# Performance work log

Measured on AMD Instinct MI355X. Metric: run time of the kernel, lower is better.

Reference implementation:

```python
import jax, jax.numpy as jnp
import numpy as np

N, H, E, T, ED, AB = 50000, 64, 800000, 800000, 64, 16


def setup_inputs() -> dict:
    key = jax.random.key(0)
    ks = jax.random.split(key, 26)

    def nrm(k, shape, scale=1.0):
        return jax.random.normal(k, shape, dtype=jnp.float32) * scale

    d = {}
    d["s"] = nrm(ks[0], (N, H))
    d["v"] = nrm(ks[1], (N, H, 3))
    d["edge_index"] = jax.random.randint(ks[2], (2, E), 0, N, dtype=jnp.int32)
    d["edge_rbf"] = jax.random.uniform(ks[3], (E, ED), dtype=jnp.float32)
    raw_dir = jax.random.normal(ks[4], (E, 3), dtype=jnp.float32)
    d["edge_dir"] = raw_dir / jnp.linalg.norm(raw_dir, axis=-1, keepdims=True)
    d["triplet_kj"] = jax.random.randint(ks[5], (T,), 0, E, dtype=jnp.int32)
    d["triplet_ji"] = jax.random.randint(ks[6], (T,), 0, E, dtype=jnp.int32)
    d["angle_feat"] = jax.random.uniform(ks[7], (T, AB), dtype=jnp.float32)

    def lin(kw, kb, fan_in, fan_out):
        sc = 1.0 / np.sqrt(fan_in)
        return nrm(kw, (fan_in, fan_out), sc), nrm(kb, (fan_out,), sc)

    d["W_t1"], d["b_t1"] = lin(ks[8], ks[9], 2 * ED + AB, H)
    d["W_t2"], d["b_t2"] = lin(ks[10], ks[11], H, H)
    d["W_m1"], d["b_m1"] = lin(ks[12], ks[13], 2 * H + ED + H, H)
    d["W_m2"], d["b_m2"] = lin(ks[14], ks[15], H, 2 * H)
    d["W_u1"], d["b_u1"] = lin(ks[16], ks[17], 3 * H, H)
    d["W_u2"], d["b_u2"] = lin(ks[18], ks[19], H, H)
    d["W_g1"], d["b_g1"] = lin(ks[20], ks[21], 3 * H, H)
    d["W_g2"], d["b_g2"] = lin(ks[22], ks[23], H, H)
    d["ln_g"] = jnp.ones((H,), jnp.float32)
    d["ln_b"] = jnp.zeros((H,), jnp.float32)
    return d


def _mlp(x, W1, b1, W2, b2):
    return jax.nn.silu(x @ W1 + b1) @ W2 + b2


def reference(s, v, edge_index, edge_rbf, edge_dir, triplet_kj, triplet_ji,
              angle_feat, W_t1, b_t1, W_t2, b_t2, W_m1, b_m1, W_m2, b_m2,
              W_u1, b_u1, W_u2, b_u2, W_g1, b_g1, W_g2, b_g2, ln_g, ln_b):
    n_nodes, hid = s.shape
    n_edges = edge_rbf.shape[0]

    # 3-body triplet messages: gather two edge rbf rows + angle feature
    t_in = jnp.concatenate([edge_rbf[triplet_kj], edge_rbf[triplet_ji], angle_feat], axis=-1)
    t_msg = _mlp(t_in, W_t1, b_t1, W_t2, b_t2)                 # [T, H]
    angle_agg = jax.ops.segment_sum(t_msg, triplet_ji, num_segments=n_edges)  # [E, H]

    src, dst = edge_index[0], edge_index[1]
    msg_in = jnp.concatenate([s[src], s[dst], edge_rbf, angle_agg], axis=-1)  # [E, 4H]
    msg = _mlp(msg_in, W_m1, b_m1, W_m2, b_m2)                 # [E, 2H]
    m_s, m_v_coeff = jnp.split(msg, 2, axis=-1)

    agg_s = jax.ops.segment_sum(m_s, dst, num_segments=n_nodes)  # [N, H]
    m_v = m_v_coeff[:, :, None] * edge_dir[:, None, :]          # [E, H, 3]
    agg_v = jax.ops.segment_sum(m_v.reshape(n_edges, hid * 3), dst,
                                num_segments=n_nodes).reshape(n_nodes, hid, 3)

    v_norm = jnp.linalg.norm(v, axis=-1)                        # [N, H]
    ctx = jnp.concatenate([s, agg_s, v_norm], axis=-1)          # [N, 3H]
    s_new = s + _mlp(ctx, W_u1, b_u1, W_u2, b_u2)
    gate = jax.nn.sigmoid(_mlp(ctx, W_g1, b_g1, W_g2, b_g2))
    v_new = v + gate[..., None] * agg_v

    mu = s_new.mean(axis=-1, keepdims=True)
    var = s_new.var(axis=-1, keepdims=True)
    s_ln = (s_new - mu) / jnp.sqrt(var + 1e-5) * ln_g + ln_b
    s_out = jax.nn.silu(s_ln)
    return (s_out, v_new)
```

## Files before the change

### kernel.cpp

```cpp
#include <hip/hip_runtime.h>
#include <cstdint>
#include <cstddef>

#define NN 50000
#define NE 800000
#define NT 800000

typedef unsigned short u16;
typedef unsigned int u32;
typedef __attribute__((ext_vector_type(8))) short short8;
typedef __attribute__((ext_vector_type(4))) float f32x4;

__device__ __forceinline__ float silu_f(float x) { return x / (1.f + __expf(-x)); }
__device__ __forceinline__ float sigm_f(float x) { return 1.f / (1.f + __expf(-x)); }
__device__ __forceinline__ u16 f2b(float x) {
  u32 u = __float_as_uint(x);
  u32 r = u + 0x7fffu + ((u >> 16) & 1u);
  return (u16)(r >> 16);
}
__device__ __forceinline__ float b2f(u16 h) { return __uint_as_float(((u32)h) << 16); }

template <int RW>
__device__ __forceinline__ int lx(int r, int c) {
  return r * RW + ((((c >> 3) ^ (r & 7)) << 3) | (c & 7));
}

__global__ __launch_bounds__(256) void kcvt2(const float* __restrict__ erbf,
                                             u16* __restrict__ erbf_bf,
                                             const float* __restrict__ s,
                                             u16* __restrict__ s_bf) {
  int i = blockIdx.x * 256 + threadIdx.x;
  const float* in;
  u16* out;
  int j;
  if (i < NE * 16) { in = erbf; out = erbf_bf; j = i; }
  else { j = i - NE * 16; if (j >= NN * 16) return; in = s; out = s_bf; }
  float4 v = ((const float4*)in)[j];
  uint2 p;
  p.x = (u32)f2b(v.x) | ((u32)f2b(v.y) << 16);
  p.y = (u32)f2b(v.z) | ((u32)f2b(v.w) << 16);
  ((uint2*)out)[j] = p;
}

__global__ __launch_bounds__(256) void khist2(const int* __restrict__ tji,
                                              const int* __restrict__ edst,
                                              int* __restrict__ tcnt,
                                              int* __restrict__ ncnt) {
  int i = blockIdx.x * 256 + threadIdx.x;
  if (i < NT) atomicAdd(&tcnt[tji[i]], 1);
  else {
    int j = i - NT;
    if (j < NE) atomicAdd(&ncnt[edst[j]], 1);
  }
}

__global__ __launch_bounds__(256) void kscan1b(
    const int* __restrict__ inA, int nA, int* __restrict__ outA, int* __restrict__ bsA, int BA,
    const int* __restrict__ inB, int nB, int* __restrict__ outB, int* __restrict__ bsB) {
  __shared__ int sh[256];
  const int* in; int n; int* out; int* bs; int blk;
  if ((int)blockIdx.x < BA) { in = inA; n = nA; out = outA; bs = bsA; blk = blockIdx.x; }
  else { in = inB; n = nB; out = outB; bs = bsB; blk = blockIdx.x - BA; }
  int tid = threadIdx.x;
  size_t base = (size_t)blk * 1024;
  int v[4];
  int acc = 0;
#pragma unroll
  for (int q = 0; q < 4; ++q) {
    size_t i = base + (size_t)tid * 4 + q;
    int x = (i < (size_t)n) ? in[i] : 0;
    v[q] = acc;
    acc += x;
  }
  sh[tid] = acc;
  __syncthreads();
  for (int off = 1; off < 256; off <<= 1) {
    int y = (tid >= off) ? sh[tid - off] : 0;
    __syncthreads();
    sh[tid] += y;
    __syncthreads();
  }
  int excl = (tid == 0) ? 0 : sh[tid - 1];
  if (tid == 255) bs[blk] = sh[255];
#pragma unroll
  for (int q = 0; q < 4; ++q) {
    size_t i = base + (size_t)tid * 4 + q;
    if (i < (size_t)n) out[i] = excl + v[q];
  }
}

__global__ __launch_bounds__(1024) void kscan2b(int* __restrict__ bsA, int nbA,
                                                int* __restrict__ bsB, int nbB) {
  __shared__ int sh[1024];
  int* bs = (blockIdx.x == 0) ? bsA : bsB;
  int nb = (blockIdx.x == 0) ? nbA : nbB;
  int tid = threadIdx.x;
  sh[tid] = (tid < nb) ? bs[tid] : 0;
  __syncthreads();
  for (int off = 1; off < 1024; off <<= 1) {
    int y = (tid >= off) ? sh[tid - off] : 0;
    __syncthreads();
    sh[tid] += y;
    __syncthreads();
  }
  if (tid < nb) bs[tid] = (tid == 0) ? 0 : sh[tid - 1];
}

__global__ __launch_bounds__(256) void kscan3b(
    int* __restrict__ outA, const int* __restrict__ bsA, int nA, int totalA,
    int* __restrict__ outB, const int* __restrict__ bsB, int nB, int totalB) {
  int i = blockIdx.x * 256 + threadIdx.x;
  if (i <= nA) {
    if (i < nA) outA[i] += bsA[i >> 10];
    else outA[nA] = totalA;
  } else {
    int j = i - (nA + 1);
    if (j < nB) outB[j] += bsB[j >> 10];
    else if (j == nB) outB[nB] = totalB;
  }
}

__global__ __launch_bounds__(256) void kscatter_inv_afeat(
    const int* __restrict__ keys, const int* __restrict__ off, int n,
    int* __restrict__ cnt, int* __restrict__ tids,
    const float* __restrict__ afeat, u16* __restrict__ afeat_s) {
  int i = blockIdx.x * 256 + threadIdx.x;
  if (i < n) {
    int k = keys[i];
    int slot = off[k] + (atomicSub(&cnt[k], 1) - 1);
    tids[slot] = i;
    const float4* src = (const float4*)(afeat + (size_t)i * 16);
    uint2* dst = (uint2*)(afeat_s + (size_t)slot * 16);
#pragma unroll
    for (int q = 0; q < 4; ++q) {
      float4 v = src[q];
      uint2 p;
      p.x = (u32)f2b(v.x) | ((u32)f2b(v.y) << 16);
      p.y = (u32)f2b(v.z) | ((u32)f2b(v.w) << 16);
      dst[q] = p;
    }
  }
}

__global__ __launch_bounds__(256) void kscatter_fwd_dir(const int* __restrict__ keys,
                                                        const int* __restrict__ off, int n,
                                                        int* __restrict__ cnt,
                                                        int* __restrict__ eids,
                                                        const float* __restrict__ dir,
                                                        float* __restrict__ dir_s) {
  int i = blockIdx.x * 256 + threadIdx.x;
  if (i < n) {
    int k = keys[i];
    int slot = off[k] + (atomicSub(&cnt[k], 1) - 1);
    eids[slot] = i;
    dir_s[(size_t)slot * 3 + 0] = dir[(size_t)i * 3 + 0];
    dir_s[(size_t)slot * 3 + 1] = dir[(size_t)i * 3 + 1];
    dir_s[(size_t)slot * 3 + 2] = dir[(size_t)i * 3 + 2];
  }
}

__global__ __launch_bounds__(256) void kprepw_all(
    const float* __restrict__ Wt1, const float* __restrict__ Wt2,
    const float* __restrict__ Wm1, const float* __restrict__ Wm2,
    const float* __restrict__ Wu1, const float* __restrict__ Wu2,
    const float* __restrict__ Wg1, const float* __restrict__ Wg2,
    u16* __restrict__ Pt1, u16* __restrict__ Pt2,
    u16* __restrict__ Pm1, u16* __restrict__ Pm2,
    u16* __restrict__ Pu1, u16* __restrict__ Pu2,
    u16* __restrict__ Pg1, u16* __restrict__ Pg2) {
  int gid = blockIdx.x * 256 + threadIdx.x;
  int f = gid >> 6, l = gid & 63;
  const float* W; u16* out; int K, N, fl;
  if (f < 20)       { W = Wt1; out = Pt1; K = 144; N = 64;  fl = f; }
  else if (f < 28)  { W = Wt2; out = Pt2; K = 64;  N = 64;  fl = f - 20; }
  else if (f < 60)  { W = Wm1; out = Pm1; K = 256; N = 64;  fl = f - 28; }
  else if (f < 76)  { W = Wm2; out = Pm2; K = 64;  N = 128; fl = f - 60; }
  else if (f < 100) { W = Wu1; out = Pu1; K = 192; N = 64;  fl = f - 76; }
  else if (f < 108) { W = Wu2; out = Pu2; K = 64;  N = 64;  fl = f - 100; }
  else if (f < 132) { W = Wg1; out = Pg1; K = 192; N = 64;  fl = f - 108; }
  else if (f < 140) { W = Wg2; out = Pg2; K = 64;  N = 64;  fl = f - 132; }
  else return;
  int nt = fl % (N / 16);
  int kt = fl / (N / 16);
  int k0 = kt * 32 + (l >> 4) * 8;
  int n = nt * 16 + (l & 15);
  u16 vals[8];
#pragma unroll
  for (int j = 0; j < 8; ++j) {
    int kk = k0 + j;
    vals[j] = (kk < K) ? f2b(W[(size_t)kk * N + n]) : (u16)0;
  }
  uint4* dst = (uint4*)(out + (size_t)fl * 512 + l * 8);
  uint4 p;
  p.x = (u32)vals[0] | ((u32)vals[1] << 16);
  p.y = (u32)vals[2] | ((u32)vals[3] << 16);
  p.z = (u32)vals[4] | ((u32)vals[5] << 16);
  p.w = (u32)vals[6] | ((u32)vals[7] << 16);
  *dst = p;
}

__global__ __launch_bounds__(256) void ktrip_mfma(
    const int* __restrict__ tkj, const int* __restrict__ tji,
    const u16* __restrict__ erbf_bf, const u16* __restrict__ afeat_s,
    const int* __restrict__ tids,
    const u16* __restrict__ Wp1, const float* __restrict__ b1,
    const u16* __restrict__ Wp2, const float* __restrict__ b2,
    u16* __restrict__ tmsg_s) {
  __shared__ u16 Xs[64 * 192];
  __shared__ u16 Hs[64 * 64];
  const int tid = threadIdx.x;
  const int l = tid & 63;
  const int w = tid >> 6;
  const int st0 = blockIdx.x * 64;

#pragma unroll
  for (int it = 0; it < 4; ++it) {
    int idx = it * 256 + tid;
    int sel = idx >> 9, r = (idx >> 3) & 63, ch = idx & 7;
    int t = tids[st0 + r];
    int node = sel ? tji[t] : tkj[t];
    uint4 vv = *(const uint4*)&erbf_bf[(size_t)node * 64 + ch * 8];
    *(uint4*)&Xs[lx<192>(r, sel * 64 + ch * 8)] = vv;
  }
  {
    int r = tid >> 2, c = (tid & 3) * 4;
    uint2 p2 = *(const uint2*)&afeat_s[(size_t)(st0 + r) * 16 + c];
    *(uint2*)&Xs[lx<192>(r, 128 + c)] = p2;
  }
#pragma unroll
  for (int i = 0; i < 2; ++i) {
    int idx = i * 256 + tid;
    int r = idx >> 3, c = 144 + (idx & 7) * 2;
    *(u32*)&Xs[lx<192>(r, c)] = 0;
  }
  __syncthreads();

  f32x4 acc1[4];
  {
    float bias = b1[w * 16 + (l & 15)];
#pragma unroll
    for (int mt = 0; mt < 4; ++mt) acc1[mt] = (f32x4){bias, bias, bias, bias};
    for (int ks = 0; ks < 5; ++ks) {
      short8 bf = *(const short8*)(Wp1 + ((size_t)(ks * 4 + w) * 64 + l) * 8);
#pragma unroll
      for (int mt = 0; mt < 4; ++mt) {
        short8 af = *(const short8*)&Xs[lx<192>(mt * 16 + (l & 15), ks * 32 + ((l >> 4) << 3))];
        acc1[mt] = __builtin_amdgcn_mfma_f32_16x16x32_bf16(af, bf, acc1[mt], 0, 0, 0);
      }
    }
  }
#pragma unroll
  for (int mt = 0; mt < 4; ++mt)
#pragma unroll
    for (int q = 0; q < 4; ++q) {
      int r = mt * 16 + (l >> 4) * 4 + q;
      Hs[lx<64>(r, w * 16 + (l & 15))] = f2b(silu_f(acc1[mt][q]));
    }
  __syncthreads();

  f32x4 acc2[4];
  {
    float bias = b2[w * 16 + (l & 15)];
#pragma unroll
    for (int mt = 0; mt < 4; ++mt) acc2[mt] = (f32x4){bias, bias, bias, bias};
    for (int ks = 0; ks < 2; ++ks) {
      short8 bf = *(const short8*)(Wp2 + ((size_t)(ks * 4 + w) * 64 + l) * 8);
#pragma unroll
      for (int mt = 0; mt < 4; ++mt) {
        short8 af = *(const short8*)&Hs[lx<64>(mt * 16 + (l & 15), ks * 32 + ((l >> 4) << 3))];
        acc2[mt] = __builtin_amdgcn_mfma_f32_16x16x32_bf16(af, bf, acc2[mt], 0, 0, 0);
      }
    }
  }
  __syncthreads();
#pragma unroll
  for (int mt = 0; mt < 4; ++mt)
#pragma unroll
    for (int q = 0; q < 4; ++q) {
      int r = mt * 16 + (l >> 4) * 4 + q;
      Xs[lx<64>(r, w * 16 + (l & 15))] = f2b(acc2[mt][q]);
    }
  __syncthreads();
  for (int i = 0; i < 2; ++i) {
    int idx = i * 256 + tid;
    int r = idx >> 3, c0 = (idx & 7) << 3;
    uint4 val = *(const uint4*)&Xs[lx<64>(r, c0)];
    *(uint4*)(tmsg_s + (size_t)(st0 + r) * 64 + c0) = val;
  }
}

__global__ __launch_bounds__(256) void kmsg_mfma(
    const int* __restrict__ eidx, const u16* __restrict__ s_bf,
    const u16* __restrict__ erbf_bf,
    const int* __restrict__ toff, const u16* __restrict__ tmsg_s,
    const int* __restrict__ eids,
    const u16* __restrict__ Wp1, const float* __restrict__ b1,
    const u16* __restrict__ Wp2, const float* __restrict__ b2,
    u16* __restrict__ msg_s) {
  __shared__ u16 Xs[64 * 256];
  __shared__ u16 Hs[64 * 64];
  const int tid = threadIdx.x;
  const int l = tid & 63;
  const int w = tid >> 6;
  const int sl0 = blockIdx.x * 64;

#pragma unroll
  for (int i = 0; i < 2; ++i) {
    int idx = i * 256 + tid;
    int r = idx >> 3, c0 = (idx & 7) << 3;
    int e = eids[sl0 + r];
    uint4 vv = *(const uint4*)&erbf_bf[(size_t)e * 64 + c0];
    *(uint4*)&Xs[lx<256>(r, 128 + c0)] = vv;
  }
#pragma unroll
  for (int it = 0; it < 4; ++it) {
    int idx = it * 256 + tid;
    int sel = idx >> 9, r = (idx >> 3) & 63, ch = idx & 7;
    int e = eids[sl0 + r];
    int node = eidx[sel * NE + e];
    uint4 vv = *(const uint4*)&s_bf[(size_t)node * 64 + ch * 8];
    *(uint4*)&Xs[lx<256>(r, sel * 64 + ch * 8)] = vv;
  }
#pragma unroll
  for (int it = 0; it < 2; ++it) {
    int idx = it * 256 + tid;
    int r = idx >> 3, ch = idx & 7;
    int e = eids[sl0 + r];
    int r0 = toff[e], r1 = toff[e + 1];
    float a[8];
#pragma unroll
    for (int j = 0; j < 8; ++j) a[j] = 0.f;
    for (int ri = r0; ri < r1; ++ri) {
      uint4 pk = *(const uint4*)&tmsg_s[(size_t)ri * 64 + ch * 8];
      a[0] += b2f((u16)(pk.x & 0xffff)); a[1] += b2f((u16)(pk.x >> 16));
      a[2] += b2f((u16)(pk.y & 0xffff)); a[3] += b2f((u16)(pk.y >> 16));
      a[4] += b2f((u16)(pk.z & 0xffff)); a[5] += b2f((u16)(pk.z >> 16));
      a[6] += b2f((u16)(pk.w & 0xffff)); a[7] += b2f((u16)(pk.w >> 16));
    }
    uint4 p;
    p.x = (u32)f2b(a[0]) | ((u32)f2b(a[1]) << 16);
    p.y = (u32)f2b(a[2]) | ((u32)f2b(a[3]) << 16);
    p.z = (u32)f2b(a[4]) | ((u32)f2b(a[5]) << 16);
    p.w = (u32)f2b(a[6]) | ((u32)f2b(a[7]) << 16);
    *(uint4*)&Xs[lx<256>(r, 192 + ch * 8)] = p;
  }
  __syncthreads();

  f32x4 acc1[4];
  {
    float bias = b1[w * 16 + (l & 15)];
#pragma unroll
    for (int mt = 0; mt < 4; ++mt) acc1[mt] = (f32x4){bias, bias, bias, bias};
    for (int ks = 0; ks < 8; ++ks) {
      short8 bf = *(const short8*)(Wp1 + ((size_t)(ks * 4 + w) * 64 + l) * 8);
#pragma unroll
      for (int mt = 0; mt < 4; ++mt) {
        short8 af = *(const short8*)&Xs[lx<256>(mt * 16 + (l & 15), ks * 32 + ((l >> 4) << 3))];
        acc1[mt] = __builtin_amdgcn_mfma_f32_16x16x32_bf16(af, bf, acc1[mt], 0, 0, 0);
      }
    }
  }
#pragma unroll
  for (int mt = 0; mt < 4; ++mt)
#pragma unroll
    for (int q = 0; q < 4; ++q) {
      int r = mt * 16 + (l >> 4) * 4 + q;
      Hs[lx<64>(r, w * 16 + (l & 15))] = f2b(silu_f(acc1[mt][q]));
    }
  __syncthreads();

  f32x4 acc2[2][4];
#pragma unroll
  for (int pp = 0; pp < 2; ++pp) {
    int nt = w * 2 + pp;
    float bias = b2[nt * 16 + (l & 15)];
#pragma unroll
    for (int mt = 0; mt < 4; ++mt) acc2[pp][mt] = (f32x4){bias, bias, bias, bias};
    for (int ks = 0; ks < 2; ++ks) {
      short8 bf = *(const short8*)(Wp2 + ((size_t)(ks * 8 + nt) * 64 + l) * 8);
#pragma unroll
      for (int mt = 0; mt < 4; ++mt) {
        short8 af = *(const short8*)&Hs[lx<64>(mt * 16 + (l & 15), ks * 32 + ((l >> 4) << 3))];
        acc2[pp][mt] = __builtin_amdgcn_mfma_f32_16x16x32_bf16(af, bf, acc2[pp][mt], 0, 0, 0);
      }
    }
  }
  __syncthreads();
#pragma unroll
  for (int pp = 0; pp < 2; ++pp)
#pragma unroll
    for (int mt = 0; mt < 4; ++mt)
#pragma unroll
      for (int q = 0; q < 4; ++q) {
        int r = mt * 16 + (l >> 4) * 4 + q;
        Xs[lx<128>(r, (w * 2 + pp) * 16 + (l & 15))] = f2b(acc2[pp][mt][q]);
      }
  __syncthreads();
  for (int i = 0; i < 4; ++i) {
    int idx = i * 256 + tid;
    int r = idx >> 4, c0 = (idx & 15) << 3;
    uint4 val = *(const uint4*)&Xs[lx<128>(r, c0)];
    *(uint4*)(msg_s + (size_t)(sl0 + r) * 128 + c0) = val;
  }
}

__global__ __launch_bounds__(256) void kagg(
    const int* __restrict__ noff, const u16* __restrict__ msg_s,
    const float* __restrict__ dir_s,
    u16* __restrict__ aggs_bf, float* __restrict__ aggv) {
  const int lane = threadIdx.x & 63;
  const int wv = threadIdx.x >> 6;
  const int n = blockIdx.x * 4 + wv;
  if (n >= NN) return;
  const int r0 = noff[n], r1 = noff[n + 1];
  const int lrow = lane >> 4, lcol = lane & 15;
  const bool is_ms = (lcol < 8);

  float a[8];
  float v0[8], v1[8], v2[8];
#pragma unroll
  for (int j = 0; j < 8; ++j) { a[j] = 0.f; v0[j] = 0.f; v1[j] = 0.f; v2[j] = 0.f; }

  for (int r4 = r0; r4 < r1; r4 += 4) {
    int r = r4 + lrow;
    if (r < r1) {
      uint4 pk = *(const uint4*)&msg_s[(size_t)r * 128 + lcol * 8];
      float x[8];
      x[0] = b2f((u16)(pk.x & 0xffff)); x[1] = b2f((u16)(pk.x >> 16));
      x[2] = b2f((u16)(pk.y & 0xffff)); x[3] = b2f((u16)(pk.y >> 16));
      x[4] = b2f((u16)(pk.z & 0xffff)); x[5] = b2f((u16)(pk.z >> 16));
      x[6] = b2f((u16)(pk.w & 0xffff)); x[7] = b2f((u16)(pk.w >> 16));
      if (is_ms) {
#pragma unroll
        for (int j = 0; j < 8; ++j) a[j] += x[j];
      } else {
        float dx = dir_s[(size_t)r * 3 + 0];
        float dy = dir_s[(size_t)r * 3 + 1];
        float dz = dir_s[(size_t)r * 3 + 2];
#pragma unroll
        for (int j = 0; j < 8; ++j) {
          v0[j] += x[j] * dx; v1[j] += x[j] * dy; v2[j] += x[j] * dz;
        }
      }
    }
  }
#pragma unroll
  for (int j = 0; j < 8; ++j) {
    a[j] += __shfl_xor(a[j], 16);  a[j] += __shfl_xor(a[j], 32);
    v0[j] += __shfl_xor(v0[j], 16); v0[j] += __shfl_xor(v0[j], 32);
    v1[j] += __shfl_xor(v1[j], 16); v1[j] += __shfl_xor(v1[j], 32);
    v2[j] += __shfl_xor(v2[j], 16); v2[j] += __shfl_xor(v2[j], 32);
  }
  if (lrow == 0) {
    if (is_ms) {
      uint4 p;
      p.x = (u32)f2b(a[0]) | ((u32)f2b(a[1]) << 16);
      p.y = (u32)f2b(a[2]) | ((u32)f2b(a[3]) << 16);
      p.z = (u32)f2b(a[4]) | ((u32)f2b(a[5]) << 16);
      p.w = (u32)f2b(a[6]) | ((u32)f2b(a[7]) << 16);
      *(uint4*)&aggs_bf[(size_t)n * 64 + lcol * 8] = p;
    } else {
      int c0 = (lcol - 8) * 8;
      float* av = aggv + (size_t)n * 192 + (size_t)c0 * 3;
      float4 o0 = {v0[0], v1[0], v2[0], v0[1]};
      float4 o1 = {v1[1], v2[1], v0[2], v1[2]};
      float4 o2 = {v2[2], v0[3], v1[3], v2[3]};
      float4 o3 = {v0[4], v1[4], v2[4], v0[5]};
      float4 o4 = {v1[5], v2[5], v0[6], v1[6]};
      float4 o5 = {v2[6], v0[7], v1[7], v2[7]};
      float4* av4 = (float4*)av;
      av4[0] = o0; av4[1] = o1; av4[2] = o2; av4[3] = o3; av4[4] = o4; av4[5] = o5;
    }
  }
}

__global__ __launch_bounds__(256) void knode_mfma(
    const u16* __restrict__ s_bf, const float* __restrict__ v,
    const u16* __restrict__ aggs_bf, const float* __restrict__ aggv,
    const u16* __restrict__ WpU1, const float* __restrict__ bU1,
    const u16* __restrict__ WpU2, const float* __restrict__ bU2,
    const u16* __restrict__ WpG1, const float* __restrict__ bG1,
    const u16* __restrict__ WpG2, const float* __restrict__ bG2,
    const float* __restrict__ lng, const float* __restrict__ lnb,
    float* __restrict__ outs, float* __restrict__ outv) {
  __shared__ __align__(16) char smem[64 * 192 * 2 + 2 * 64 * 64 * 2];
  u16* Xs = (u16*)smem;
  u16* Hu = (u16*)(smem + 64 * 192 * 2);
  u16* Hg = Hu + 64 * 64;
  float* Fs = (float*)smem;

  const int tid = threadIdx.x;
  const int l = tid & 63;
  const int w = tid >> 6;
  const int n0 = blockIdx.x * 64;

  for (int i = 0; i < 2; ++i) {
    int idx = i * 256 + tid;
    int r = idx >> 3, c0 = (idx & 7) << 3;
    int nr = n0 + r; if (nr >= NN) nr = NN - 1;
    uint4 a = *(const uint4*)&s_bf[(size_t)nr * 64 + c0];
    *(uint4*)&Xs[lx<192>(r, c0)] = a;
    uint4 b = *(const uint4*)&aggs_bf[(size_t)nr * 64 + c0];
    *(uint4*)&Xs[lx<192>(r, 64 + c0)] = b;
  }
  for (int it = 0; it < 16; ++it) {
    int idx = it * 256 + tid;
    int r = idx >> 6, c = idx & 63;
    int nr = n0 + r; if (nr >= NN) nr = NN - 1;
    const float* vp = v + (size_t)nr * 192 + c * 3;
    float x = vp[0], y = vp[1], z = vp[2];
    Xs[lx<192>(r, 128 + c)] = f2b(sqrtf(x * x + y * y + z * z));
  }
  __syncthreads();

  f32x4 au[4], ag[4];
  {
    float biu = bU1[w * 16 + (l & 15)], big = bG1[w * 16 + (l & 15)];
#pragma unroll
    for (int mt = 0; mt < 4; ++mt) {
      au[mt] = (f32x4){biu, biu, biu, biu};
      ag[mt] = (f32x4){big, big, big, big};
    }
    for (int ks = 0; ks < 6; ++ks) {
      short8 bu = *(const short8*)(WpU1 + ((size_t)(ks * 4 + w) * 64 + l) * 8);
      short8 bg = *(const short8*)(WpG1 + ((size_t)(ks * 4 + w) * 64 + l) * 8);
#pragma unroll
      for (int mt = 0; mt < 4; ++mt) {
        short8 af = *(const short8*)&Xs[lx<192>(mt * 16 + (l & 15), ks * 32 + ((l >> 4) << 3))];
        au[mt] = __builtin_amdgcn_mfma_f32_16x16x32_bf16(af, bu, au[mt], 0, 0, 0);
        ag[mt] = __builtin_amdgcn_mfma_f32_16x16x32_bf16(af, bg, ag[mt], 0, 0, 0);
      }
    }
  }
#pragma unroll
  for (int mt = 0; mt < 4; ++mt)
#pragma unroll
    for (int q = 0; q < 4; ++q) {
      int r = mt * 16 + (l >> 4) * 4 + q;
      Hu[lx<64>(r, w * 16 + (l & 15))] = f2b(silu_f(au[mt][q]));
      Hg[lx<64>(r, w * 16 + (l & 15))] = f2b(silu_f(ag[mt][q]));
    }
  __syncthreads();

  f32x4 ou[4], og[4];
  {
    float biu = bU2[w * 16 + (l & 15)], big = bG2[w * 16 + (l & 15)];
#pragma unroll
    for (int mt = 0; mt < 4; ++mt) {
      ou[mt] = (f32x4){biu, biu, biu, biu};
      og[mt] = (f32x4){big, big, big, big};
    }
    for (int ks = 0; ks < 2; ++ks) {
      short8 bu = *(const short8*)(WpU2 + ((size_t)(ks * 4 + w) * 64 + l) * 8);
      short8 bg = *(const short8*)(WpG2 + ((size_t)(ks * 4 + w) * 64 + l) * 8);
#pragma unroll
      for (int mt = 0; mt < 4; ++mt) {
        short8 afu = *(const short8*)&Hu[lx<64>(mt * 16 + (l & 15), ks * 32 + ((l >> 4) << 3))];
        ou[mt] = __builtin_amdgcn_mfma_f32_16x16x32_bf16(afu, bu, ou[mt], 0, 0, 0);
        short8 afg = *(const short8*)&Hg[lx<64>(mt * 16 + (l & 15), ks * 32 + ((l >> 4) << 3))];
        og[mt] = __builtin_amdgcn_mfma_f32_16x16x32_bf16(afg, bg, og[mt], 0, 0, 0);
      }
    }
  }
#pragma unroll
  for (int mt = 0; mt < 4; ++mt)
#pragma unroll
    for (int q = 0; q < 4; ++q) {
      int r = mt * 16 + (l >> 4) * 4 + q;
      ou[mt][q] += b2f(Xs[lx<192>(r, w * 16 + (l & 15))]);
    }
  __syncthreads();

#pragma unroll
  for (int mt = 0; mt < 4; ++mt)
#pragma unroll
    for (int q = 0; q < 4; ++q) {
      int r = mt * 16 + (l >> 4) * 4 + q;
      Fs[r * 68 + w * 16 + (l & 15)] = ou[mt][q];
    }
  __syncthreads();
  {
    int r = tid >> 2, c0 = (tid & 3) * 16;
    float xv[16];
#pragma unroll
    for (int j4 = 0; j4 < 4; ++j4) {
      float4 t = *(const float4*)&Fs[r * 68 + c0 + j4 * 4];
      xv[j4 * 4 + 0] = t.x; xv[j4 * 4 + 1] = t.y;
      xv[j4 * 4 + 2] = t.z; xv[j4 * 4 + 3] = t.w;
    }
    float sm = 0.f, sq = 0.f;
#pragma unroll
    for (int j = 0; j < 16; ++j) { sm += xv[j]; sq += xv[j] * xv[j]; }
    sm += __shfl_xor(sm, 1); sq += __shfl_xor(sq, 1);
    sm += __shfl_xor(sm, 2); sq += __shfl_xor(sq, 2);
    float mu = sm * (1.f / 64.f);
    float var = sq * (1.f / 64.f) - mu * mu;
    float rstd = rsqrtf(var + 1e-5f);
    if (n0 + r < NN) {
      float* op = outs + (size_t)(n0 + r) * 64 + c0;
#pragma unroll
      for (int j4 = 0; j4 < 4; ++j4) {
        float4 o;
        float y0 = (xv[j4 * 4 + 0] - mu) * rstd * lng[c0 + j4 * 4 + 0] + lnb[c0 + j4 * 4 + 0];
        float y1 = (xv[j4 * 4 + 1] - mu) * rstd * lng[c0 + j4 * 4 + 1] + lnb[c0 + j4 * 4 + 1];
        float y2 = (xv[j4 * 4 + 2] - mu) * rstd * lng[c0 + j4 * 4 + 2] + lnb[c0 + j4 * 4 + 2];
        float y3 = (xv[j4 * 4 + 3] - mu) * rstd * lng[c0 + j4 * 4 + 3] + lnb[c0 + j4 * 4 + 3];
        o.x = silu_f(y0); o.y = silu_f(y1); o.z = silu_f(y2); o.w = silu_f(y3);
        *(float4*)(op + j4 * 4) = o;
      }
    }
  }
  __syncthreads();

#pragma unroll
  for (int mt = 0; mt < 4; ++mt)
#pragma unroll
    for (int q = 0; q < 4; ++q) {
      int r = mt * 16 + (l >> 4) * 4 + q;
      Fs[r * 68 + w * 16 + (l & 15)] = og[mt][q];
    }
  __syncthreads();
  {
    int r = tid >> 2, c0 = (tid & 3) * 16;
    int nr = n0 + r;
    if (nr < NN) {
      float gate[16];
#pragma unroll
      for (int j = 0; j < 16; ++j) gate[j] = sigm_f(Fs[r * 68 + c0 + j]);
      const float4* vp = (const float4*)(v + (size_t)nr * 192 + c0 * 3);
      const float4* ap = (const float4*)(aggv + (size_t)nr * 192 + c0 * 3);
      float4* op = (float4*)(outv + (size_t)nr * 192 + c0 * 3);
#pragma unroll
      for (int j4 = 0; j4 < 12; ++j4) {
        float4 vv = vp[j4], av = ap[j4], o;
        o.x = vv.x + gate[(j4 * 4 + 0) / 3] * av.x;
        o.y = vv.y + gate[(j4 * 4 + 1) / 3] * av.y;
        o.z = vv.z + gate[(j4 * 4 + 2) / 3] * av.z;
        o.w = vv.w + gate[(j4 * 4 + 3) / 3] * av.w;
        op[j4] = o;
      }
    }
  }
}

extern "C" void kernel_launch(void* const* d_in, const int* in_sizes, int n_in,
                              void* d_out, int out_size, void* d_ws, size_t ws_size,
                              hipStream_t stream) {
  const float* s     = (const float*)d_in[0];
  const float* v     = (const float*)d_in[1];
  const int*   eidx  = (const int*)d_in[2];
  const float* erbf  = (const float*)d_in[3];
  const float* edir  = (const float*)d_in[4];
  const int*   tkj   = (const int*)d_in[5];
  const int*   tji   = (const int*)d_in[6];
  const float* afeat = (const float*)d_in[7];
  const float* W_t1  = (const float*)d_in[8];
  const float* b_t1  = (const float*)d_in[9];
  const float* W_t2  = (const float*)d_in[10];
  const float* b_t2  = (const float*)d_in[11];
  const float* W_m1  = (const float*)d_in[12];
  const float* b_m1  = (const float*)d_in[13];
  const float* W_m2  = (const float*)d_in[14];
  const float* b_m2  = (const float*)d_in[15];
  const float* W_u1  = (const float*)d_in[16];
  const float* b_u1  = (const float*)d_in[17];
  const float* W_u2  = (const float*)d_in[18];
  const float* b_u2  = (const float*)d_in[19];
  const float* W_g1  = (const float*)d_in[20];
  const float* b_g1  = (const float*)d_in[21];
  const float* W_g2  = (const float*)d_in[22];
  const float* b_g2  = (const float*)d_in[23];
  const float* ln_g  = (const float*)d_in[24];
  const float* ln_b  = (const float*)d_in[25];

  char* w = (char*)d_ws;
  auto alloc = [&](size_t bytes) -> char* {
    char* p = w;
    w += (bytes + 255) & ~(size_t)255;
    return p;
  };
  int* toff  = (int*)alloc((size_t)(NE + 1) * 4);
  int* noff  = (int*)alloc((size_t)(NN + 1) * 4);
  int* tcnt  = (int*)alloc((size_t)NE * 4);
  int* ncnt  = (int*)alloc((size_t)NN * 4);
  int* tids  = (int*)alloc((size_t)NT * 4);
  int* eids  = (int*)alloc((size_t)NE * 4);
  int* bsum  = (int*)alloc(2048 * 4);
  float* dir_s = (float*)alloc((size_t)NE * 3 * 4);
  u16* msg_s  = (u16*)alloc((size_t)NE * 128 * 2);
  u16* tmsg_s = (u16*)alloc((size_t)NT * 64 * 2);
  u16* erbf_bf = (u16*)alloc((size_t)NE * 64 * 2);
  u16* s_bf    = (u16*)alloc((size_t)NN * 64 * 2);
  u16* Wp_t1 = (u16*)alloc((size_t)5 * 4 * 512 * 2);
  u16* Wp_t2 = (u16*)alloc((size_t)2 * 4 * 512 * 2);
  u16* Wp_m1 = (u16*)alloc((size_t)8 * 4 * 512 * 2);
  u16* Wp_m2 = (u16*)alloc((size_t)2 * 8 * 512 * 2);
  u16* Wp_u1 = (u16*)alloc((size_t)6 * 4 * 512 * 2);
  u16* Wp_u2 = (u16*)alloc((size_t)2 * 4 * 512 * 2);
  u16* Wp_g1 = (u16*)alloc((size_t)6 * 4 * 512 * 2);
  u16* Wp_g2 = (u16*)alloc((size_t)2 * 4 * 512 * 2);
  u16* afeat_s = msg_s;
  float* aggv = (float*)tmsg_s;
  u16* aggs_bf = tmsg_s + (size_t)NN * 384;

  hipMemsetAsync(tcnt, 0, (size_t)((char*)(ncnt + NN) - (char*)tcnt), stream);

  kcvt2<<<(NE * 16 + NN * 16 + 255) / 256, 256, 0, stream>>>(erbf, erbf_bf, s, s_bf);
  khist2<<<(NT + NE + 255) / 256, 256, 0, stream>>>(tji, eidx + NE, tcnt, ncnt);

  const int Bt = (NE + 1023) / 1024, Bn = (NN + 1023) / 1024;
  kscan1b<<<Bt + Bn, 256, 0, stream>>>(tcnt, NE, toff, bsum, Bt, ncnt, NN, noff, bsum + 1024);
  kscan2b<<<2, 1024, 0, stream>>>(bsum, Bt, bsum + 1024, Bn);
  kscan3b<<<(NE + 1 + NN + 1 + 255) / 256, 256, 0, stream>>>(toff, bsum, NE, NT,
                                                             noff, bsum + 1024, NN, NE);

  kscatter_inv_afeat<<<(NT + 255) / 256, 256, 0, stream>>>(tji, toff, NT, tcnt, tids,
                                                           afeat, afeat_s);
  kscatter_fwd_dir<<<(NE + 255) / 256, 256, 0, stream>>>(eidx + NE, noff, NE, ncnt, eids,
                                                         edir, dir_s);

  kprepw_all<<<35, 256, 0, stream>>>(W_t1, W_t2, W_m1, W_m2, W_u1, W_u2, W_g1, W_g2,
                                     Wp_t1, Wp_t2, Wp_m1, Wp_m2, Wp_u1, Wp_u2, Wp_g1, Wp_g2);

  ktrip_mfma<<<NT / 64, 256, 0, stream>>>(tkj, tji, erbf_bf, afeat_s, tids,
                                          Wp_t1, b_t1, Wp_t2, b_t2, tmsg_s);
  kmsg_mfma<<<NE / 64, 256, 0, stream>>>(eidx, s_bf, erbf_bf, toff, tmsg_s, eids,
                                         Wp_m1, b_m1, Wp_m2, b_m2, msg_s);
  kagg<<<(NN + 3) / 4, 256, 0, stream>>>(noff, msg_s, dir_s, aggs_bf, aggv);

  float* out_s = (float*)d_out;
  float* out_v = out_s + (size_t)NN * 64;
  knode_mfma<<<(NN + 63) / 64, 256, 0, stream>>>(s_bf, v, aggs_bf, aggv,
                                                 Wp_u1, b_u1, Wp_u2, b_u2,
                                                 Wp_g1, b_g1, Wp_g2, b_g2,
                                                 ln_g, ln_b, out_s, out_v);
}
```

Measured before the change: 643.5 us.

## Merge prep kernels and process edges in original order with scattered message writes

Fuses conversion with the histogram kernel, and merges the two scatter kernels with weight packing into one launch, cutting launch count. The message kernel now walks edges in their natural order, so its erbf/edge_index/toff reads are contiguous. It writes each output row to that edge's dst-sorted slot through a new eslot array, replacing the earlier gather through eids. This trades indirect reads for indirect 256-byte row writes.

New measurement: 618.1 us. 4.0% less time.

```diff
diff --git a/kernel.cpp b/kernel.cpp
--- a/kernel.cpp
+++ b/kernel.cpp
@@ -19,38 +19,38 @@
   return (u16)(r >> 16);
 }
 __device__ __forceinline__ float b2f(u16 h) { return __uint_as_float(((u32)h) << 16); }
+__device__ __forceinline__ u32 pk2(float a, float b) {
+  return (u32)f2b(a) | ((u32)f2b(b) << 16);
+}
 
 template <int RW>
 __device__ __forceinline__ int lx(int r, int c) {
   return r * RW + ((((c >> 3) ^ (r & 7)) << 3) | (c & 7));
 }
 
-__global__ __launch_bounds__(256) void kcvt2(const float* __restrict__ erbf,
-                                             u16* __restrict__ erbf_bf,
-                                             const float* __restrict__ s,
-                                             u16* __restrict__ s_bf) {
+__global__ __launch_bounds__(256) void kcvt_hist(
+    const float* __restrict__ erbf, u16* __restrict__ erbf_bf,
+    const float* __restrict__ s, u16* __restrict__ s_bf,
+    const int* __restrict__ tji, const int* __restrict__ edst,
+    int* __restrict__ tcnt, int* __restrict__ ncnt) {
   int i = blockIdx.x * 256 + threadIdx.x;
-  const float* in;
-  u16* out;
-  int j;
-  if (i < NE * 16) { in = erbf; out = erbf_bf; j = i; }
-  else { j = i - NE * 16; if (j >= NN * 16) return; in = s; out = s_bf; }
-  float4 v = ((const float4*)in)[j];
-  uint2 p;
-  p.x = (u32)f2b(v.x) | ((u32)f2b(v.y) << 16);
-  p.y = (u32)f2b(v.z) | ((u32)f2b(v.w) << 16);
-  ((uint2*)out)[j] = p;
-}
-
-__global__ __launch_bounds__(256) void khist2(const int* __restrict__ tji,
-                                              const int* __restrict__ edst,
-                                              int* __restrict__ tcnt,
-                                              int* __restrict__ ncnt) {
-  int i = blockIdx.x * 256 + threadIdx.x;
-  if (i < NT) atomicAdd(&tcnt[tji[i]], 1);
-  else {
-    int j = i - NT;
-    if (j < NE) atomicAdd(&ncnt[edst[j]], 1);
+  const int NCVT = (NE + NN) * 16;
+  if (i < NCVT) {
+    const float* in; u16* out; int j;
+    if (i < NE * 16) { in = erbf; out = erbf_bf; j = i; }
+    else { in = s; out = s_bf; j = i - NE * 16; }
+    float4 v = ((const float4*)in)[j];
+    uint2 p;
+    p.x = pk2(v.x, v.y);
+    p.y = pk2(v.z, v.w);
+    ((uint2*)out)[j] = p;
+  } else {
+    int j = i - NCVT;
+    if (j < NT) atomicAdd(&tcnt[tji[j]], 1);
+    else {
+      j -= NT;
+      if (j < NE) atomicAdd(&ncnt[edst[j]], 1);
+    }
   }
 }
 
@@ -120,46 +120,11 @@
   }
 }
 
-__global__ __launch_bounds__(256) void kscatter_inv_afeat(
-    const int* __restrict__ keys, const int* __restrict__ off, int n,
-    int* __restrict__ cnt, int* __restrict__ tids,
-    const float* __restrict__ afeat, u16* __restrict__ afeat_s) {
-  int i = blockIdx.x * 256 + threadIdx.x;
-  if (i < n) {
-    int k = keys[i];
-    int slot = off[k] + (atomicSub(&cnt[k], 1) - 1);
-    tids[slot] = i;
-    const float4* src = (const float4*)(afeat + (size_t)i * 16);
-    uint2* dst = (uint2*)(afeat_s + (size_t)slot * 16);
-#pragma unroll
-    for (int q = 0; q < 4; ++q) {
-      float4 v = src[q];
-      uint2 p;
-      p.x = (u32)f2b(v.x) | ((u32)f2b(v.y) << 16);
-      p.y = (u32)f2b(v.z) | ((u32)f2b(v.w) << 16);
-      dst[q] = p;
-    }
-  }
-}
-
-__global__ __launch_bounds__(256) void kscatter_fwd_dir(const int* __restrict__ keys,
-                                                        const int* __restrict__ off, int n,
-                                                        int* __restrict__ cnt,
-                                                        int* __restrict__ eids,
-                                                        const float* __restrict__ dir,
-                                                        float* __restrict__ dir_s) {
-  int i = blockIdx.x * 256 + threadIdx.x;
-  if (i < n) {
-    int k = keys[i];
-    int slot = off[k] + (atomicSub(&cnt[k], 1) - 1);
-    eids[slot] = i;
-    dir_s[(size_t)slot * 3 + 0] = dir[(size_t)i * 3 + 0];
-    dir_s[(size_t)slot * 3 + 1] = dir[(size_t)i * 3 + 1];
-    dir_s[(size_t)slot * 3 + 2] = dir[(size_t)i * 3 + 2];
-  }
-}
-
-__global__ __launch_bounds__(256) void kprepw_all(
+__global__ __launch_bounds__(256) void kprep_all(
+    const int* __restrict__ tji, const int* __restrict__ toff, int* __restrict__ tcnt,
+    int* __restrict__ tids, const float* __restrict__ afeat, u16* __restrict__ afeat_s,
+    const int* __restrict__ edst, const int* __restrict__ noff, int* __restrict__ ncnt,
+    int* __restrict__ eslot, const float* __restrict__ dir, float* __restrict__ dir_s,
     const float* __restrict__ Wt1, const float* __restrict__ Wt2,
     const float* __restrict__ Wm1, const float* __restrict__ Wm2,
     const float* __restrict__ Wu1, const float* __restrict__ Wu2,
@@ -168,35 +133,60 @@
     u16* __restrict__ Pm1, u16* __restrict__ Pm2,
     u16* __restrict__ Pu1, u16* __restrict__ Pu2,
     u16* __restrict__ Pg1, u16* __restrict__ Pg2) {
-  int gid = blockIdx.x * 256 + threadIdx.x;
-  int f = gid >> 6, l = gid & 63;
-  const float* W; u16* out; int K, N, fl;
-  if (f < 20)       { W = Wt1; out = Pt1; K = 144; N = 64;  fl = f; }
-  else if (f < 28)  { W = Wt2; out = Pt2; K = 64;  N = 64;  fl = f - 20; }
-  else if (f < 60)  { W = Wm1; out = Pm1; K = 256; N = 64;  fl = f - 28; }
-  else if (f < 76)  { W = Wm2; out = Pm2; K = 64;  N = 128; fl = f - 60; }
-  else if (f < 100) { W = Wu1; out = Pu1; K = 192; N = 64;  fl = f - 76; }
-  else if (f < 108) { W = Wu2; out = Pu2; K = 64;  N = 64;  fl = f - 100; }
-  else if (f < 132) { W = Wg1; out = Pg1; K = 192; N = 64;  fl = f - 108; }
-  else if (f < 140) { W = Wg2; out = Pg2; K = 64;  N = 64;  fl = f - 132; }
-  else return;
-  int nt = fl % (N / 16);
-  int kt = fl / (N / 16);
-  int k0 = kt * 32 + (l >> 4) * 8;
-  int n = nt * 16 + (l & 15);
-  u16 vals[8];
-#pragma unroll
-  for (int j = 0; j < 8; ++j) {
-    int kk = k0 + j;
-    vals[j] = (kk < K) ? f2b(W[(size_t)kk * N + n]) : (u16)0;
-  }
-  uint4* dst = (uint4*)(out + (size_t)fl * 512 + l * 8);
-  uint4 p;
-  p.x = (u32)vals[0] | ((u32)vals[1] << 16);
-  p.y = (u32)vals[2] | ((u32)vals[3] << 16);
-  p.z = (u32)vals[4] | ((u32)vals[5] << 16);
-  p.w = (u32)vals[6] | ((u32)vals[7] << 16);
-  *dst = p;
+  int i = blockIdx.x * 256 + threadIdx.x;
+  if (i < NT) {
+    int k = tji[i];
+    int slot = toff[k] + (atomicSub(&tcnt[k], 1) - 1);
+    tids[slot] = i;
+    const float4* src = (const float4*)(afeat + (size_t)i * 16);
+    uint2* dst = (uint2*)(afeat_s + (size_t)slot * 16);
+#pragma unroll
+    for (int q = 0; q < 4; ++q) {
+      float4 v = src[q];
+      uint2 p;
+      p.x = pk2(v.x, v.y);
+      p.y = pk2(v.z, v.w);
+      dst[q] = p;
+    }
+  } else if (i < NT + NE) {
+    int j = i - NT;
+    int k = edst[j];
+    int slot = noff[k] + (atomicSub(&ncnt[k], 1) - 1);
+    eslot[j] = slot;
+    dir_s[(size_t)slot * 3 + 0] = dir[(size_t)j * 3 + 0];
+    dir_s[(size_t)slot * 3 + 1] = dir[(size_t)j * 3 + 1];
+    dir_s[(size_t)slot * 3 + 2] = dir[(size_t)j * 3 + 2];
+  } else {
+    int g = i - NT - NE;
+    int f = g >> 6, l = g & 63;
+    const float* W; u16* out; int K, N, fl;
+    if (f < 20)       { W = Wt1; out = Pt1; K = 144; N = 64;  fl = f; }
+    else if (f < 28)  { W = Wt2; out = Pt2; K = 64;  N = 64;  fl = f - 20; }
+    else if (f < 60)  { W = Wm1; out = Pm1; K = 256; N = 64;  fl = f - 28; }
+    else if (f < 76)  { W = Wm2; out = Pm2; K = 64;  N = 128; fl = f - 60; }
+    else if (f < 100) { W = Wu1; out = Pu1; K = 192; N = 64;  fl = f - 76; }
+    else if (f < 108) { W = Wu2; out = Pu2; K = 64;  N = 64;  fl = f - 100; }
+    else if (f < 132) { W = Wg1; out = Pg1; K = 192; N = 64;  fl = f - 108; }
+    else if (f < 140) { W = Wg2; out = Pg2; K = 64;  N = 64;  fl = f - 132; }
+    else return;
+    int nt = fl % (N / 16);
+    int kt = fl / (N / 16);
+    int k0 = kt * 32 + (l >> 4) * 8;
+    int n = nt * 16 + (l & 15);
+    u16 vals[8];
+#pragma unroll
+    for (int j = 0; j < 8; ++j) {
+      int kk = k0 + j;
+      vals[j] = (kk < K) ? f2b(W[(size_t)kk * N + n]) : (u16)0;
+    }
+    uint4* dst = (uint4*)(out + (size_t)fl * 512 + l * 8);
+    uint4 p;
+    p.x = (u32)vals[0] | ((u32)vals[1] << 16);
+    p.y = (u32)vals[2] | ((u32)vals[3] << 16);
+    p.z = (u32)vals[4] | ((u32)vals[5] << 16);
+    p.w = (u32)vals[6] | ((u32)vals[7] << 16);
+    *dst = p;
+  }
 }
 
 __global__ __launch_bounds__(256) void ktrip_mfma(
@@ -293,7 +283,7 @@
     const int* __restrict__ eidx, const u16* __restrict__ s_bf,
     const u16* __restrict__ erbf_bf,
     const int* __restrict__ toff, const u16* __restrict__ tmsg_s,
-    const int* __restrict__ eids,
+    const int* __restrict__ eslot,
     const u16* __restrict__ Wp1, const float* __restrict__ b1,
     const u16* __restrict__ Wp2, const float* __restrict__ b2,
     u16* __restrict__ msg_s) {
@@ -302,22 +292,20 @@
   const int tid = threadIdx.x;
   const int l = tid & 63;
   const int w = tid >> 6;
-  const int sl0 = blockIdx.x * 64;
+  const int e0 = blockIdx.x * 64;
 
 #pragma unroll
   for (int i = 0; i < 2; ++i) {
     int idx = i * 256 + tid;
     int r = idx >> 3, c0 = (idx & 7) << 3;
-    int e = eids[sl0 + r];
-    uint4 vv = *(const uint4*)&erbf_bf[(size_t)e * 64 + c0];
+    uint4 vv = *(const uint4*)&erbf_bf[(size_t)(e0 + r) * 64 + c0];
     *(uint4*)&Xs[lx<256>(r, 128 + c0)] = vv;
   }
 #pragma unroll
   for (int it = 0; it < 4; ++it) {
     int idx = it * 256 + tid;
     int sel = idx >> 9, r = (idx >> 3) & 63, ch = idx & 7;
-    int e = eids[sl0 + r];
-    int node = eidx[sel * NE + e];
+    int node = eidx[sel * NE + e0 + r];
     uint4 vv = *(const uint4*)&s_bf[(size_t)node * 64 + ch * 8];
     *(uint4*)&Xs[lx<256>(r, sel * 64 + ch * 8)] = vv;
   }
@@ -325,7 +313,7 @@
   for (int it = 0; it < 2; ++it) {
     int idx = it * 256 + tid;
     int r = idx >> 3, ch = idx & 7;
-    int e = eids[sl0 + r];
+    int e = e0 + r;
     int r0 = toff[e], r1 = toff[e + 1];
     float a[8];
 #pragma unroll
@@ -338,10 +326,10 @@
       a[6] += b2f((u16)(pk.w & 0xffff)); a[7] += b2f((u16)(pk.w >> 16));
     }
     uint4 p;
-    p.x = (u32)f2b(a[0]) | ((u32)f2b(a[1]) << 16);
-    p.y = (u32)f2b(a[2]) | ((u32)f2b(a[3]) << 16);
-    p.z = (u32)f2b(a[4]) | ((u32)f2b(a[5]) << 16);
-    p.w = (u32)f2b(a[6]) | ((u32)f2b(a[7]) << 16);
+    p.x = pk2(a[0], a[1]);
+    p.y = pk2(a[2], a[3]);
+    p.z = pk2(a[4], a[5]);
+    p.w = pk2(a[6], a[7]);
     *(uint4*)&Xs[lx<256>(r, 192 + ch * 8)] = p;
   }
   __syncthreads();
@@ -399,8 +387,9 @@
   for (int i = 0; i < 4; ++i) {
     int idx = i * 256 + tid;
     int r = idx >> 4, c0 = (idx & 15) << 3;
+    int slot = eslot[e0 + r];
     uint4 val = *(const uint4*)&Xs[lx<128>(r, c0)];
-    *(uint4*)(msg_s + (size_t)(sl0 + r) * 128 + c0) = val;
+    *(uint4*)(msg_s + (size_t)slot * 128 + c0) = val;
   }
 }
 
@@ -454,10 +443,10 @@
   if (lrow == 0) {
     if (is_ms) {
       uint4 p;
-      p.x = (u32)f2b(a[0]) | ((u32)f2b(a[1]) << 16);
-      p.y = (u32)f2b(a[2]) | ((u32)f2b(a[3]) << 16);
-      p.z = (u32)f2b(a[4]) | ((u32)f2b(a[5]) << 16);
-      p.w = (u32)f2b(a[6]) | ((u32)f2b(a[7]) << 16);
+      p.x = pk2(a[0], a[1]);
+      p.y = pk2(a[2], a[3]);
+      p.z = pk2(a[4], a[5]);
+      p.w = pk2(a[6], a[7]);
       *(uint4*)&aggs_bf[(size_t)n * 64 + lcol * 8] = p;
     } else {
       int c0 = (lcol - 8) * 8;
@@ -679,12 +668,13 @@
     w += (bytes + 255) & ~(size_t)255;
     return p;
   };
+  int* tcnt  = (int*)alloc((size_t)NE * 4);
+  int* ncnt  = (int*)alloc((size_t)NN * 4);
+  size_t zspan = (size_t)((char*)(ncnt + NN) - (char*)tcnt);
   int* toff  = (int*)alloc((size_t)(NE + 1) * 4);
   int* noff  = (int*)alloc((size_t)(NN + 1) * 4);
-  int* tcnt  = (int*)alloc((size_t)NE * 4);
-  int* ncnt  = (int*)alloc((size_t)NN * 4);
   int* tids  = (int*)alloc((size_t)NT * 4);
-  int* eids  = (int*)alloc((size_t)NE * 4);
+  int* eslot = (int*)alloc((size_t)NE * 4);
   int* bsum  = (int*)alloc(2048 * 4);
   float* dir_s = (float*)alloc((size_t)NE * 3 * 4);
   u16* msg_s  = (u16*)alloc((size_t)NE * 128 * 2);
@@ -703,10 +693,10 @@
   float* aggv = (float*)tmsg_s;
   u16* aggs_bf = tmsg_s + (size_t)NN * 384;
 
-  hipMemsetAsync(tcnt, 0, (size_t)((char*)(ncnt + NN) - (char*)tcnt), stream);
-
-  kcvt2<<<(NE * 16 + NN * 16 + 255) / 256, 256, 0, stream>>>(erbf, erbf_bf, s, s_bf);
-  khist2<<<(NT + NE + 255) / 256, 256, 0, stream>>>(tji, eidx + NE, tcnt, ncnt);
+  hipMemsetAsync(tcnt, 0, zspan, stream);
+
+  kcvt_hist<<<((NE + NN) * 16 + NT + NE + 255) / 256, 256, 0, stream>>>(
+      erbf, erbf_bf, s, s_bf, tji, eidx + NE, tcnt, ncnt);
 
   const int Bt = (NE + 1023) / 1024, Bn = (NN + 1023) / 1024;
   kscan1b<<<Bt + Bn, 256, 0, stream>>>(tcnt, NE, toff, bsum, Bt, ncnt, NN, noff, bsum + 1024);
@@ -714,17 +704,15 @@
   kscan3b<<<(NE + 1 + NN + 1 + 255) / 256, 256, 0, stream>>>(toff, bsum, NE, NT,
                                                              noff, bsum + 1024, NN, NE);
 
-  kscatter_inv_afeat<<<(NT + 255) / 256, 256, 0, stream>>>(tji, toff, NT, tcnt, tids,
-                                                           afeat, afeat_s);
-  kscatter_fwd_dir<<<(NE + 255) / 256, 256, 0, stream>>>(eidx + NE, noff, NE, ncnt, eids,
-                                                         edir, dir_s);
-
-  kprepw_all<<<35, 256, 0, stream>>>(W_t1, W_t2, W_m1, W_m2, W_u1, W_u2, W_g1, W_g2,
-                                     Wp_t1, Wp_t2, Wp_m1, Wp_m2, Wp_u1, Wp_u2, Wp_g1, Wp_g2);
+  kprep_all<<<(NT + NE + 140 * 64 + 255) / 256, 256, 0, stream>>>(
+      tji, toff, tcnt, tids, afeat, afeat_s,
+      eidx + NE, noff, ncnt, eslot, edir, dir_s,
+      W_t1, W_t2, W_m1, W_m2, W_u1, W_u2, W_g1, W_g2,
+      Wp_t1, Wp_t2, Wp_m1, Wp_m2, Wp_u1, Wp_u2, Wp_g1, Wp_g2);
 
   ktrip_mfma<<<NT / 64, 256, 0, stream>>>(tkj, tji, erbf_bf, afeat_s, tids,
                                           Wp_t1, b_t1, Wp_t2, b_t2, tmsg_s);
-  kmsg_mfma<<<NE / 64, 256, 0, stream>>>(eidx, s_bf, erbf_bf, toff, tmsg_s, eids,
+  kmsg_mfma<<<NE / 64, 256, 0, stream>>>(eidx, s_bf, erbf_bf, toff, tmsg_s, eslot,
                                          Wp_m1, b_m1, Wp_m2, b_m2, msg_s);
   kagg<<<(NN + 3) / 4, 256, 0, stream>>>(noff, msg_s, dir_s, aggs_bf, aggv);
 
```
